# Kernel optimization log

Measured on AMD Instinct MI355X. Metric: run time of the kernel, lower is better.

## Reference

```python
import jax, jax.numpy as jnp
import numpy as np

B, K, C, Q, NCLS = 16, 36, 2048, 1024, 16
LIN = 1024
DIN = 2 * C + 16 + Q  # 5136


def _linear_params(key, din, dout, scale=0.02):
    kw, kb = jax.random.split(key)
    W = jax.random.normal(kw, (din, dout), dtype=jnp.float32) * scale
    b = jax.random.normal(kb, (dout,), dtype=jnp.float32) * scale
    return W, b


def setup_inputs() -> dict:
    key = jax.random.key(0)
    ks = jax.random.split(key, 12)
    box_feats = jax.random.normal(ks[0], (B, K, C), dtype=jnp.float32)
    q_feats = jax.random.normal(ks[1], (B, Q), dtype=jnp.float32)
    # valid boxes: x2>x1, y2>y1 so areas are strictly positive (no div-by-zero)
    x1y1 = jax.random.uniform(ks[2], (B, K, 2), dtype=jnp.float32)
    wh = jax.random.uniform(ks[3], (B, K, 2), dtype=jnp.float32, minval=0.05, maxval=1.0)
    box_coords = jnp.concatenate([x1y1, x1y1 + wh, wh], axis=-1)  # [B,K,6]
    index = jax.random.randint(ks[4], (B,), 1, K + 1)  # ragged box counts in [1,K]
    wholefeat = jax.random.normal(ks[5], (B, C), dtype=jnp.float32)
    pooled = jax.random.normal(ks[6], (B, C), dtype=jnp.float32)
    W1, b1 = _linear_params(ks[7], DIN, LIN)
    W2, b2 = _linear_params(ks[8], LIN, LIN)
    W3, b3 = _linear_params(ks[9], LIN, LIN)
    Wf1, bf1 = _linear_params(ks[10], LIN, LIN // 2)
    Wf2, bf2 = _linear_params(ks[11], LIN // 2, NCLS)
    return {"wholefeat": wholefeat, "pooled": pooled, "box_feats": box_feats,
            "q_feats": q_feats, "box_coords": box_coords, "index": index,
            "W1": W1, "b1": b1, "W2": W2, "b2": b2, "W3": W3, "b3": b3,
            "Wf1": Wf1, "bf1": bf1, "Wf2": Wf2, "bf2": bf2}


def _rn_forward(box_feats, q_feats, box_coords, index,
                W1, b1, W2, b2, W3, b3, Wf1, bf1, Wf2, bf2):
    b_, k_, c_ = box_feats.shape
    # ragged -> padded + mask: pair (i,j) valid iff i < index[b] and j < index[b]
    valid = (jnp.arange(k_)[None, :] < index[:, None]).astype(box_feats.dtype)  # [B,K]
    pair_mask = valid[:, :, None] * valid[:, None, :]  # [B,K,K]

    # pairwise dot of region features
    dot = jnp.einsum('bid,bjd->bij', box_feats, box_feats)[..., None]  # [B,K,K,1]

    bc = box_coords  # [B,K,6]
    area = (bc[..., 2] - bc[..., 0]) * (bc[..., 3] - bc[..., 1])  # [B,K]
    lr = jnp.maximum(0.0, jnp.minimum(bc[:, :, None, 2], bc[:, None, :, 2])
                     - jnp.maximum(bc[:, :, None, 0], bc[:, None, :, 0]))
    ud = jnp.maximum(0.0, jnp.minimum(bc[:, :, None, 3], bc[:, None, :, 3])
                     - jnp.maximum(bc[:, :, None, 1], bc[:, None, :, 1]))
    overlap = lr * ud  # [B,K,K]
    area_i = area[:, :, None]
    area_j = area[:, None, :]
    iou = (overlap / (area_i + area_j - overlap))[..., None]
    o_ij = (overlap / area_i)[..., None]
    o_ji = (overlap / area_j)[..., None]

    b_ij = jnp.broadcast_to(bc[:, :, None, :], (b_, k_, k_, 6))
    b_ji = jnp.broadcast_to(bc[:, None, :, :], (b_, k_, k_, 6))
    o_i = jnp.broadcast_to(box_feats[:, :, None, :], (b_, k_, k_, c_))
    o_j = jnp.broadcast_to(box_feats[:, None, :, :], (b_, k_, k_, c_))
    qst = jnp.broadcast_to(q_feats[:, None, None, :], (b_, k_, k_, q_feats.shape[-1]))

    # [B,K,K,5136] = [o_i, o_j, qst, dot, b_ij, b_ji, iou, o_ij, o_ji]
    feat = jnp.concatenate([o_i, o_j, qst, dot, b_ij, b_ji, iou, o_ij, o_ji], axis=-1)

    h = jax.nn.relu(feat @ W1 + b1)
    h = jax.nn.relu(h @ W2 + b2)
    h = jax.nn.relu(h @ W3 + b3)  # [B,K,K,1024]

    # masked sum-pool over all valid (i,j) pairs
    g = jnp.einsum('bijh,bij->bh', h, pair_mask)  # [B,1024]

    out = jax.nn.relu(g @ Wf1 + bf1) @ Wf2 + bf2  # [B,Ncls]
    return out


def reference(wholefeat, pooled, box_feats, q_feats, box_coords, index,
              W1, b1, W2, b2, W3, b3, Wf1, bf1, Wf2, bf2):
    # wholefeat / pooled are unused by the original forward as well
    return _rn_forward(box_feats, q_feats, box_coords, index,
                       W1, b1, W2, b2, W3, b3, Wf1, bf1, Wf2, bf2)
```

## Files before the change

kernel.cpp:

```cpp
#include <hip/hip_runtime.h>
#include <stdint.h>

typedef unsigned short u16;
typedef __attribute__((ext_vector_type(8))) short short8;
typedef __attribute__((ext_vector_type(4))) float f32x4;

#define Bn 16
#define Kn 36
#define Cn 2048
#define Qn 1024
#define LINn 1024
#define NPp 1296
#define NPAIRn 20736
#define NBIn 576

__device__ __forceinline__ u16 f2bf(float f) {
  union { float f; unsigned int u; } v; v.f = f;
  unsigned int r = v.u + 0x7FFFu + ((v.u >> 16) & 1u);
  return (u16)(r >> 16);
}

__device__ __forceinline__ void llds16(const void* g, void* l) {
  __builtin_amdgcn_global_load_lds((const __attribute__((address_space(1))) void*)g,
                                   (__attribute__((address_space(3))) void*)l, 16, 0, 0);
}

__global__ void k_transpose_all(const float* __restrict__ W1, const float* __restrict__ W2,
                                const float* __restrict__ W3, u16* __restrict__ W1abT,
                                u16* __restrict__ W2T, u16* __restrict__ W3T) {
  __shared__ float tile[32][33];
  int z = blockIdx.z;
  const float* src; u16* dst; int ld_dst;
  if (z == 0)      { if (blockIdx.y >= 32) return; src = W2; dst = W2T; ld_dst = 1024; }
  else if (z == 1) { if (blockIdx.y >= 32) return; src = W3; dst = W3T; ld_dst = 1024; }
  else if (z == 2) { src = W1; dst = W1abT; ld_dst = 2048; }
  else             { src = W1 + (size_t)2048 * 1024; dst = W1abT + (size_t)1024 * 2048; ld_dst = 2048; }
  int n0 = blockIdx.x * 32, k0 = blockIdx.y * 32;
  int tx = threadIdx.x & 31, ty = threadIdx.x >> 5;
#pragma unroll
  for (int r = 0; r < 32; r += 8)
    tile[ty + r][tx] = src[(size_t)(k0 + ty + r) * 1024 + (n0 + tx)];
  __syncthreads();
#pragma unroll
  for (int r = 0; r < 32; r += 8)
    dst[(size_t)(n0 + ty + r) * ld_dst + (k0 + tx)] = f2bf(tile[tx][ty + r]);
}

__global__ void k_f2b(const float4* __restrict__ src, ushort4* __restrict__ dst, int n4) {
  int i = blockIdx.x * 256 + threadIdx.x;
  if (i < n4) {
    float4 v = src[i];
    ushort4 o;
    o.x = f2bf(v.x); o.y = f2bf(v.y); o.z = f2bf(v.z); o.w = f2bf(v.w);
    dst[i] = o;
  }
}

__global__ void k_build(const int* __restrict__ index, int* __restrict__ pairList,
                        int* __restrict__ batchC, int* __restrict__ cnt2) {
  __shared__ int offs[17];
  int tid = threadIdx.x;
  if (tid == 0) {
    int o = 0;
    for (int b = 0; b < Bn; ++b) { offs[b] = o; int v = index[b]; o += v * v; }
    offs[16] = o;
    cnt2[0] = o;
    cnt2[1] = (o + 127) & ~127;
  }
  __syncthreads();
  int total = offs[16];
  int totalPad = (total + 127) & ~127;
  for (int b = 0; b < Bn; ++b) {
    int v = index[b]; int n = v * v; int base = offs[b];
    for (int t = tid; t < n; t += 256) {
      int i = t / v, j = t - i * v;
      pairList[base + t] = b * NPp + i * Kn + j;
      batchC[base + t] = b;
    }
  }
  for (int t = total + tid; t < totalPad; t += 256) {
    pairList[t] = 0;
    batchC[t] = 0;
  }
}

__global__ void k_pcinit(const float* __restrict__ b1, float* __restrict__ Pc) {
  int n = blockIdx.x * 256 + threadIdx.x;
  float v = b1[n];
#pragma unroll
  for (int b = 0; b < Bn; ++b) Pc[b * LINn + n] = v;
}

__global__ void k_pconst(const float* __restrict__ q, const float* __restrict__ W1,
                         float* __restrict__ Pc) {
  __shared__ float qs[Bn][32];
  int n = blockIdx.x * 256 + threadIdx.x;
  int k0 = blockIdx.y * 32;
  const float* Wq = W1 + (size_t)(2 * Cn) * LINn;
  for (int t = threadIdx.x; t < Bn * 32; t += 256) {
    int b = t >> 5, k = t & 31;
    qs[b][k] = q[b * Qn + k0 + k];
  }
  __syncthreads();
  float acc[Bn];
#pragma unroll
  for (int b = 0; b < Bn; ++b) acc[b] = 0.f;
  for (int k = 0; k < 32; ++k) {
    float w = Wq[(size_t)(k0 + k) * LINn + n];
#pragma unroll
    for (int b = 0; b < Bn; ++b) acc[b] += qs[b][k] * w;
  }
#pragma unroll
  for (int b = 0; b < Bn; ++b) atomicAdd(&Pc[b * LINn + n], acc[b]);
}

__global__ void k_pairscalars(const float* __restrict__ bfm, const float* __restrict__ bc,
                              const int* __restrict__ pairList, const int* __restrict__ cnt2,
                              float* __restrict__ dotC, float* __restrict__ iouC,
                              float* __restrict__ oijC, float* __restrict__ ojiC) {
  int cnt = cnt2[0];
  int lane = threadIdx.x & 63;
  for (int m = blockIdx.x * 4 + (threadIdx.x >> 6); m < cnt; m += gridDim.x * 4) {
    int p = pairList[m];
    int b = p / NPp, rem = p - b * NPp, i = rem / Kn, j = rem - (rem / Kn) * Kn;
    const float4* Ai = (const float4*)(bfm + (size_t)(b * Kn + i) * Cn);
    const float4* Aj = (const float4*)(bfm + (size_t)(b * Kn + j) * Cn);
    float s = 0.f;
#pragma unroll
    for (int t = 0; t < Cn / 4 / 64; ++t) {
      float4 x = Ai[lane + t * 64], y = Aj[lane + t * 64];
      s += x.x * y.x + x.y * y.y + x.z * y.z + x.w * y.w;
    }
#pragma unroll
    for (int o = 32; o > 0; o >>= 1) s += __shfl_down(s, o);
    if (lane == 0) {
      const float* ci = bc + (size_t)(b * Kn + i) * 6;
      const float* cj = bc + (size_t)(b * Kn + j) * 6;
      float ai = (ci[2] - ci[0]) * (ci[3] - ci[1]);
      float aj = (cj[2] - cj[0]) * (cj[3] - cj[1]);
      float lr = fmaxf(0.f, fminf(ci[2], cj[2]) - fmaxf(ci[0], cj[0]));
      float ud = fmaxf(0.f, fminf(ci[3], cj[3]) - fmaxf(ci[1], cj[1]));
      float ov = lr * ud;
      dotC[m] = s;
      iouC[m] = ov / (ai + aj - ov);
      oijC[m] = ov / ai;
      ojiC[m] = ov / aj;
    }
  }
}

__global__ void k_padd(const float* __restrict__ P12s, const float* __restrict__ Pc,
                       const float* __restrict__ bc, const float* __restrict__ W1,
                       float* __restrict__ P12) {
  int bi = blockIdx.x;
  int b = bi / Kn;
  const float* c = bc + (size_t)bi * 6;
  const float* W = W1 + (size_t)(2 * Cn + Qn + 1) * LINn;
  const size_t SL = (size_t)640 * 2048;
#pragma unroll
  for (int it = 0; it < 8; ++it) {
    int cc = it * 256 + threadIdx.x;
    size_t idx = (size_t)bi * 2048 + cc;
    float s = P12s[idx] + P12s[SL + idx] + P12s[2 * SL + idx] + P12s[3 * SL + idx];
    int n = cc & 1023;
    int rbase = (cc < 1024) ? 0 : 6;
    float a = 0.f;
#pragma unroll
    for (int t = 0; t < 6; ++t) a += c[t] * W[(size_t)(rbase + t) * LINn + n];
    if (cc < 1024) a += Pc[b * LINn + n];
    P12[idx] = s + a;
  }
}

__global__ void k_h1(const float* __restrict__ P12,
                     const float* __restrict__ dotC, const float* __restrict__ iouC,
                     const float* __restrict__ oijC, const float* __restrict__ ojiC,
                     const int* __restrict__ pairList, const int* __restrict__ cnt2,
                     const float* __restrict__ W1, u16* __restrict__ H1) {
  int cnt = cnt2[0];
  int t = threadIdx.x;
  const float4* wd = (const float4*)(W1 + (size_t)(2 * Cn + Qn) * LINn);
  const float4* wu = (const float4*)(W1 + (size_t)(2 * Cn + Qn + 13) * LINn);
  const float4* wa = (const float4*)(W1 + (size_t)(2 * Cn + Qn + 14) * LINn);
  const float4* wb = (const float4*)(W1 + (size_t)(2 * Cn + Qn + 15) * LINn);
  float4 e1 = wd[t], e2 = wu[t], e3 = wa[t], e4 = wb[t];
  for (int m = blockIdx.x; m < cnt; m += gridDim.x) {
    int p = pairList[m];
    int b = p / NPp, rem = p - b * NPp, i = rem / Kn, j = rem - (rem / Kn) * Kn;
    float d = dotC[m], u = iouC[m], o1 = oijC[m], o2 = ojiC[m];
    const float4* p1 = (const float4*)(P12 + (size_t)(b * Kn + i) * 2048);
    const float4* p2 = (const float4*)(P12 + (size_t)(b * Kn + j) * 2048 + 1024);
    ushort4* outp = (ushort4*)(H1 + (size_t)m * 1024);
    float4 v1 = p1[t], v2 = p2[t];
    ushort4 o;
    o.x = f2bf(fmaxf(v1.x + v2.x + d * e1.x + u * e2.x + o1 * e3.x + o2 * e4.x, 0.f));
    o.y = f2bf(fmaxf(v1.y + v2.y + d * e1.y + u * e2.y + o1 * e3.y + o2 * e4.y, 0.f));
    o.z = f2bf(fmaxf(v1.z + v2.z + d * e1.z + u * e2.z + o1 * e3.z + o2 * e4.z, 0.f));
    o.w = f2bf(fmaxf(v1.w + v2.w + d * e1.w + u * e2.w + o1 * e3.w + o2 * e4.w, 0.f));
    outp[t] = o;
  }
}

template <int EPI>
__global__ void __launch_bounds__(256) k_gemm(
    const u16* __restrict__ A, const u16* __restrict__ BT,
    int N, int K, int KC, int Mvalid, const int* __restrict__ cnt2,
    float* __restrict__ Cf, int CfSlice, u16* __restrict__ Cb,
    const float* __restrict__ bias,
    const int* __restrict__ batchC, float* __restrict__ G) {
  __shared__ u16 Alds[2][128 * 32];
  __shared__ u16 Blds[2][64 * 32];
  __shared__ float Gpart[(EPI == 2) ? (Bn * 64) : 4];

  const int tid = threadIdx.x;
  const int wave = tid >> 6, lane = tid & 63;
  const int wm = (wave >> 1) * 64, wn = (wave & 1) * 32;

  int Mv = Mvalid;
  int m0, n0;
  if (EPI == 0) {
    m0 = blockIdx.x * 128;
    n0 = blockIdx.y * 64;
  } else {
    Mv = cnt2[0];
    int nMt = (Mv + 127) >> 7;
    int nact = nMt * 16;
    int id = blockIdx.x;
    if (id >= nact) return;
    int q = nact >> 3, r = nact & 7;
    int xcd = id & 7, rank = id >> 3;
    int wg = (xcd < r ? xcd * (q + 1) : r * (q + 1) + (xcd - r) * q) + rank;
    m0 = (wg >> 4) * 128;
    n0 = (wg & 15) * 64;
  }
  if (EPI == 2) {
    for (int t = tid; t < Bn * 64; t += 256) Gpart[t] = 0.f;
  }

  f32x4 zero = {0.f, 0.f, 0.f, 0.f};
  f32x4 acc[4][2];
#pragma unroll
  for (int x = 0; x < 4; ++x)
#pragma unroll
    for (int y = 0; y < 2; ++y) acc[x][y] = zero;

  const int arow = tid >> 2;
  const int sslot = ((tid & 3) ^ ((tid >> 3) & 3)) * 16;
  const size_t ldb = (size_t)K * 2;

  auto stage = [&](int buf, int k0) {
    char* aB = (char*)Alds[buf] + wave * 1024;
    char* bB = (char*)Blds[buf] + wave * 1024;
#pragma unroll
    for (int c = 0; c < 2; ++c) {
      int rg = m0 + c * 64 + arow; if (rg >= Mv) rg = Mv - 1;
      llds16((const char*)A + (size_t)rg * ldb + (size_t)k0 * 2 + sslot, aB + c * 4096);
    }
    int rg = n0 + arow;
    llds16((const char*)BT + (size_t)rg * ldb + (size_t)k0 * 2 + sslot, bB);
  };

  auto compute = [&](int buf) {
    const char* Ab = (const char*)Alds[buf];
    const char* Bb = (const char*)Blds[buf];
    short8 af[4], bfr[2];
#pragma unroll
    for (int f = 0; f < 4; ++f) {
      int rA = wm + f * 16 + (lane & 15);
      int sl = ((lane >> 4) ^ ((rA >> 1) & 3)) * 16;
      af[f] = *(const short8*)(Ab + (size_t)rA * 64 + sl);
    }
#pragma unroll
    for (int f = 0; f < 2; ++f) {
      int rB = wn + f * 16 + (lane & 15);
      int sl = ((lane >> 4) ^ ((rB >> 1) & 3)) * 16;
      bfr[f] = *(const short8*)(Bb + (size_t)rB * 64 + sl);
    }
#pragma unroll
    for (int x = 0; x < 4; ++x)
#pragma unroll
      for (int y = 0; y < 2; ++y)
        acc[x][y] = __builtin_amdgcn_mfma_f32_16x16x32_bf16(af[x], bfr[y],
                                                            acc[x][y], 0, 0, 0);
  };

  const int kbeg = blockIdx.z * KC;
  const int nt = KC >> 5;
  stage(0, kbeg);
  for (int t = 0; t < nt; ++t) {
    if (t + 1 < nt) {
      stage((t + 1) & 1, kbeg + (t + 1) * 32);
      asm volatile("s_waitcnt vmcnt(3)" ::: "memory");
    } else {
      asm volatile("s_waitcnt vmcnt(0)" ::: "memory");
    }
    __builtin_amdgcn_s_barrier();
    compute(t & 1);
    __builtin_amdgcn_s_barrier();
  }

  if (EPI == 0) {
    float* Cs = Cf + (size_t)blockIdx.z * CfSlice;
#pragma unroll
    for (int x = 0; x < 4; ++x) {
      int rb = m0 + wm + x * 16 + (lane >> 4) * 4;
#pragma unroll
      for (int r = 0; r < 4; ++r) {
        int row = rb + r;
        if (row < Mv) {
#pragma unroll
          for (int y = 0; y < 2; ++y)
            Cs[(size_t)row * N + (n0 + wn + y * 16 + (lane & 15))] = acc[x][y][r];
        }
      }
    }
  } else if (EPI == 1) {
#pragma unroll
    for (int x = 0; x < 4; ++x) {
      int rb = m0 + wm + x * 16 + (lane >> 4) * 4;
#pragma unroll
      for (int r = 0; r < 4; ++r) {
        int row = rb + r;
#pragma unroll
        for (int y = 0; y < 2; ++y) {
          int col = n0 + wn + y * 16 + (lane & 15);
          Cb[(size_t)row * N + col] = f2bf(fmaxf(acc[x][y][r] + bias[col], 0.f));
        }
      }
    }
  } else {
    const int cnt = Mv;
#pragma unroll
    for (int x = 0; x < 4; ++x) {
      int rb = m0 + wm + x * 16 + (lane >> 4) * 4;
      int b0 = batchC[rb], b1 = batchC[rb + 1], b2 = batchC[rb + 2], b3 = batchC[rb + 3];
      float mk0 = (rb     < cnt) ? 1.f : 0.f;
      float mk1 = (rb + 1 < cnt) ? 1.f : 0.f;
      float mk2 = (rb + 2 < cnt) ? 1.f : 0.f;
      float mk3 = (rb + 3 < cnt) ? 1.f : 0.f;
#pragma unroll
      for (int y = 0; y < 2; ++y) {
        int coll = wn + y * 16 + (lane & 15);
        float bs = bias[n0 + coll];
        float s0 = mk0 * fmaxf(acc[x][y][0] + bs, 0.f);
        float s1 = mk1 * fmaxf(acc[x][y][1] + bs, 0.f);
        float s2 = mk2 * fmaxf(acc[x][y][2] + bs, 0.f);
        float s3 = mk3 * fmaxf(acc[x][y][3] + bs, 0.f);
        if (b0 == b3) {
          atomicAdd(&Gpart[b0 * 64 + coll], s0 + s1 + s2 + s3);
        } else {
          atomicAdd(&Gpart[b0 * 64 + coll], s0);
          atomicAdd(&Gpart[b1 * 64 + coll], s1);
          atomicAdd(&Gpart[b2 * 64 + coll], s2);
          atomicAdd(&Gpart[b3 * 64 + coll], s3);
        }
      }
    }
    __syncthreads();
    for (int t2 = tid; t2 < Bn * 64; t2 += 256) {
      float v = Gpart[t2];
      if (v != 0.f) atomicAdd(&G[(t2 >> 6) * LINn + n0 + (t2 & 63)], v);
    }
  }
}

__global__ void k_final1(const float* __restrict__ G, const float* __restrict__ Wf1,
                         float* __restrict__ S) {
  __shared__ float g[128];
  int b = blockIdx.x, kz = blockIdx.y, tid = threadIdx.x;
  if (tid < 128) g[tid] = G[b * 1024 + kz * 128 + tid];
  __syncthreads();
  float acc = 0.f;
  const float* W = Wf1 + (size_t)(kz * 128) * 512 + tid;
  for (int k = 0; k < 128; ++k) acc += g[k] * W[(size_t)k * 512];
  atomicAdd(&S[b * 512 + tid], acc);
}

__global__ void k_final2(const float* __restrict__ S, const float* __restrict__ bf1,
                         const float* __restrict__ Wf2, const float* __restrict__ bf2,
                         float* __restrict__ out) {
  __shared__ float mid[512];
  __shared__ float part[256];
  int b = blockIdx.x, tid = threadIdx.x;
  for (int t = tid; t < 512; t += 256) mid[t] = fmaxf(S[b * 512 + t] + bf1[t], 0.f);
  __syncthreads();
  int o = tid & 15, seg = tid >> 4;
  float s = 0.f;
#pragma unroll
  for (int t = 0; t < 32; ++t) {
    int j = seg * 32 + t;
    s += mid[j] * Wf2[j * 16 + o];
  }
  part[tid] = s;
  __syncthreads();
  if (tid < 16) {
    float v = bf2[tid];
#pragma unroll
    for (int sg = 0; sg < 16; ++sg) v += part[sg * 16 + tid];
    out[b * 16 + tid] = v;
  }
}

extern "C" void kernel_launch(void* const* d_in, const int* in_sizes, int n_in,
                              void* d_out, int out_size, void* d_ws, size_t ws_size,
                              hipStream_t stream) {
  const float* box_feats  = (const float*)d_in[2];
  const float* q_feats    = (const float*)d_in[3];
  const float* box_coords = (const float*)d_in[4];
  const int*   index      = (const int*)d_in[5];
  const float* W1  = (const float*)d_in[6];
  const float* b1  = (const float*)d_in[7];
  const float* W2  = (const float*)d_in[8];
  const float* b2  = (const float*)d_in[9];
  const float* W3  = (const float*)d_in[10];
  const float* b3  = (const float*)d_in[11];
  const float* Wf1 = (const float*)d_in[12];
  const float* bf1 = (const float*)d_in[13];
  const float* Wf2 = (const float*)d_in[14];
  const float* bf2 = (const float*)d_in[15];
  float* out = (float*)d_out;

  char* ws = (char*)d_ws;
  size_t off = 0;
  auto alloc = [&](size_t bytes) { void* p = ws + off; off += (bytes + 255) & ~(size_t)255; return p; };
  u16* W1abT = (u16*)alloc((size_t)2048 * 2048 * 2);
  u16* W2T   = (u16*)alloc((size_t)1024 * 1024 * 2);
  u16* W3T   = (u16*)alloc((size_t)1024 * 1024 * 2);
  u16* BFb   = (u16*)alloc((size_t)NBIn * Cn * 2);
  float* P12s = (float*)alloc((size_t)4 * 640 * 2048 * 4);
  float* P12  = (float*)alloc((size_t)NBIn * 2048 * 4);
  float* Pc   = (float*)alloc((size_t)Bn * LINn * 4);
  float* dotC = (float*)alloc((size_t)NPAIRn * 4);
  float* iouC = (float*)alloc((size_t)NPAIRn * 4);
  float* oijC = (float*)alloc((size_t)NPAIRn * 4);
  float* ojiC = (float*)alloc((size_t)NPAIRn * 4);
  int* pairList = (int*)alloc((size_t)NPAIRn * 4);
  int* batchC   = (int*)alloc((size_t)NPAIRn * 4);
  int* cnt2     = (int*)alloc(64);
  float* G  = (float*)alloc((size_t)Bn * LINn * 4);
  float* S  = (float*)alloc((size_t)Bn * 512 * 4);
  u16* H1 = (u16*)alloc((size_t)NPAIRn * 1024 * 2);
  u16* H2 = (u16*)alloc((size_t)NPAIRn * 1024 * 2);

  k_transpose_all<<<dim3(32, 64, 4), 256, 0, stream>>>(W1, W2, W3, W1abT, W2T, W3T);
  k_f2b<<<(NBIn * Cn / 4 + 255) / 256, 256, 0, stream>>>((const float4*)box_feats,
                                                         (ushort4*)BFb, NBIn * Cn / 4);
  k_build<<<1, 256, 0, stream>>>(index, pairList, batchC, cnt2);
  k_pcinit<<<4, 256, 0, stream>>>(b1, Pc);
  k_pconst<<<dim3(4, 32), 256, 0, stream>>>(q_feats, W1, Pc);
  k_pairscalars<<<648, 256, 0, stream>>>(box_feats, box_coords, pairList, cnt2,
                                         dotC, iouC, oijC, ojiC);
  k_gemm<0><<<dim3(5, 32, 4), 256, 0, stream>>>(BFb, W1abT, 2048, 2048, 512, NBIn, nullptr,
                                                P12s, 640 * 2048, nullptr, nullptr,
                                                nullptr, nullptr);
  k_padd<<<NBIn, 256, 0, stream>>>(P12s, Pc, box_coords, W1, P12);
  k_h1<<<2592, 256, 0, stream>>>(P12, dotC, iouC, oijC, ojiC, pairList, cnt2, W1, H1);
  hipMemsetAsync(G, 0, (size_t)Bn * LINn * 4, stream);
  hipMemsetAsync(S, 0, (size_t)Bn * 512 * 4, stream);
  k_gemm<1><<<dim3(2592, 1, 1), 256, 0, stream>>>(H1, W2T, 1024, 1024, 1024, 0, cnt2,
                                                  nullptr, 0, H2, b2, nullptr, nullptr);
  k_gemm<2><<<dim3(2592, 1, 1), 256, 0, stream>>>(H2, W3T, 1024, 1024, 1024, 0, cnt2,
                                                  nullptr, 0, nullptr, b3, batchC, G);
  k_final1<<<dim3(16, 8), 512, 0, stream>>>(G, Wf1, S);
  k_final2<<<16, 256, 0, stream>>>(S, bf1, Wf2, bf2, out);
}
```

Baseline: 159.3 us.

## Fuse second and third MLP GEMMs into one kernel keeping activations in LDS

Replaces the two separate GEMM launches for layers 2 and 3 with one kernel. Each 512-thread block holds a 64-row tile of H1 in LDS (128KB), computes all 1024 output columns of layer 2, writes the ReLU'd bf16 result back into the same LDS tile, then runs layer 3 and sum-pools straight into G with global atomics. This removes the H2 round trip through HBM and one launch. In exchange, weight B-fragments are loaded directly from global memory without LDS staging, each block gets only 64 rows of reuse, per-thread accumulator pressure is high, and the shared-LDS partial reduction is replaced by direct global atomics.

```diff
diff --git a/kernel.cpp b/kernel.cpp
--- a/kernel.cpp
+++ b/kernel.cpp
@@ -201,41 +201,18 @@
   }
 }
 
-template <int EPI>
-__global__ void __launch_bounds__(256) k_gemm(
+__global__ void __launch_bounds__(256) k_gemmP(
     const u16* __restrict__ A, const u16* __restrict__ BT,
-    int N, int K, int KC, int Mvalid, const int* __restrict__ cnt2,
-    float* __restrict__ Cf, int CfSlice, u16* __restrict__ Cb,
-    const float* __restrict__ bias,
-    const int* __restrict__ batchC, float* __restrict__ G) {
+    int N, int K, int KC, int Mvalid,
+    float* __restrict__ Cf, int CfSlice) {
   __shared__ u16 Alds[2][128 * 32];
   __shared__ u16 Blds[2][64 * 32];
-  __shared__ float Gpart[(EPI == 2) ? (Bn * 64) : 4];
-
   const int tid = threadIdx.x;
   const int wave = tid >> 6, lane = tid & 63;
   const int wm = (wave >> 1) * 64, wn = (wave & 1) * 32;
-
-  int Mv = Mvalid;
-  int m0, n0;
-  if (EPI == 0) {
-    m0 = blockIdx.x * 128;
-    n0 = blockIdx.y * 64;
-  } else {
-    Mv = cnt2[0];
-    int nMt = (Mv + 127) >> 7;
-    int nact = nMt * 16;
-    int id = blockIdx.x;
-    if (id >= nact) return;
-    int q = nact >> 3, r = nact & 7;
-    int xcd = id & 7, rank = id >> 3;
-    int wg = (xcd < r ? xcd * (q + 1) : r * (q + 1) + (xcd - r) * q) + rank;
-    m0 = (wg >> 4) * 128;
-    n0 = (wg & 15) * 64;
-  }
-  if (EPI == 2) {
-    for (int t = tid; t < Bn * 64; t += 256) Gpart[t] = 0.f;
-  }
+  const int m0 = blockIdx.x * 128;
+  const int n0 = blockIdx.y * 64;
+  const int Mv = Mvalid;
 
   f32x4 zero = {0.f, 0.f, 0.f, 0.f};
   f32x4 acc[4][2];
@@ -299,67 +276,152 @@
     __builtin_amdgcn_s_barrier();
   }
 
-  if (EPI == 0) {
-    float* Cs = Cf + (size_t)blockIdx.z * CfSlice;
-#pragma unroll
-    for (int x = 0; x < 4; ++x) {
-      int rb = m0 + wm + x * 16 + (lane >> 4) * 4;
+  float* Cs = Cf + (size_t)blockIdx.z * CfSlice;
+#pragma unroll
+  for (int x = 0; x < 4; ++x) {
+    int rb = m0 + wm + x * 16 + (lane >> 4) * 4;
+#pragma unroll
+    for (int r = 0; r < 4; ++r) {
+      int row = rb + r;
+      if (row < Mv) {
+#pragma unroll
+        for (int y = 0; y < 2; ++y)
+          Cs[(size_t)row * N + (n0 + wn + y * 16 + (lane & 15))] = acc[x][y][r];
+      }
+    }
+  }
+}
+
+__global__ void __launch_bounds__(512, 2) k_fused23(
+    const u16* __restrict__ H1, const u16* __restrict__ W2T, const u16* __restrict__ W3T,
+    const float* __restrict__ b2, const float* __restrict__ b3,
+    const int* __restrict__ batchC, const int* __restrict__ cnt2,
+    float* __restrict__ G) {
+  __shared__ u16 T[64][1024];
+  const int tid = threadIdx.x;
+  const int wave = tid >> 6, lane = tid & 63;
+  const int cnt = cnt2[0];
+  const int r0g = blockIdx.x * 64;
+  if (r0g >= cnt) return;
+  const int cw = wave * 128;
+
+#pragma unroll
+  for (int rd = 0; rd < 16; ++rd) {
+    int row = rd * 4 + (wave >> 1);
+    int s0 = (wave & 1) << 6;
+    int gr = r0g + row; if (gr >= cnt) gr = cnt - 1;
+    int sslot = (s0 + lane) ^ (row & 7);
+    llds16(H1 + (size_t)gr * 1024 + (size_t)sslot * 8, &T[row][s0 * 8]);
+  }
+  __syncthreads();
+
+  f32x4 zero = {0.f, 0.f, 0.f, 0.f};
+  f32x4 acc[4][8];
+#pragma unroll
+  for (int x = 0; x < 4; ++x)
+#pragma unroll
+    for (int y = 0; y < 8; ++y) acc[x][y] = zero;
+
+  float bias[8];
+#pragma unroll
+  for (int y = 0; y < 8; ++y) bias[y] = b2[cw + y * 16 + (lane & 15)];
+
+#pragma unroll 2
+  for (int k0 = 0; k0 < 1024; k0 += 64) {
+#pragma unroll
+    for (int kk = 0; kk < 2; ++kk) {
+      int ksl = (k0 >> 3) + kk * 4 + (lane >> 4);
+      short8 af[4];
+#pragma unroll
+      for (int x = 0; x < 4; ++x) {
+        int row = x * 16 + (lane & 15);
+        af[x] = *(const short8*)&T[row][(ksl ^ (row & 7)) << 3];
+      }
+      const u16* wp = W2T + k0 + kk * 32 + ((lane >> 4) << 3);
+      short8 bf[8];
+#pragma unroll
+      for (int y = 0; y < 8; ++y)
+        bf[y] = *(const short8*)(wp + (size_t)(cw + y * 16 + (lane & 15)) * 1024);
+#pragma unroll
+      for (int x = 0; x < 4; ++x)
+#pragma unroll
+        for (int y = 0; y < 8; ++y)
+          acc[x][y] = __builtin_amdgcn_mfma_f32_16x16x32_bf16(af[x], bf[y],
+                                                              acc[x][y], 0, 0, 0);
+    }
+  }
+
+  __syncthreads();
+#pragma unroll
+  for (int x = 0; x < 4; ++x) {
+    int rbase = x * 16 + ((lane >> 4) << 2);
+#pragma unroll
+    for (int y = 0; y < 8; ++y) {
+      int col = cw + y * 16 + (lane & 15);
 #pragma unroll
       for (int r = 0; r < 4; ++r) {
-        int row = rb + r;
-        if (row < Mv) {
-#pragma unroll
-          for (int y = 0; y < 2; ++y)
-            Cs[(size_t)row * N + (n0 + wn + y * 16 + (lane & 15))] = acc[x][y][r];
-        }
+        int row = rbase + r;
+        float v = fmaxf(acc[x][y][r] + bias[y], 0.f);
+        T[row][((((col >> 3) ^ (row & 7)) << 3) | (col & 7))] = f2bf(v);
       }
-    }
-  } else if (EPI == 1) {
-#pragma unroll
-    for (int x = 0; x < 4; ++x) {
-      int rb = m0 + wm + x * 16 + (lane >> 4) * 4;
-#pragma unroll
-      for (int r = 0; r < 4; ++r) {
-        int row = rb + r;
-#pragma unroll
-        for (int y = 0; y < 2; ++y) {
-          int col = n0 + wn + y * 16 + (lane & 15);
-          Cb[(size_t)row * N + col] = f2bf(fmaxf(acc[x][y][r] + bias[col], 0.f));
-        }
+      acc[x][y] = zero;
+    }
+  }
+  __syncthreads();
+
+#pragma unroll
+  for (int y = 0; y < 8; ++y) bias[y] = b3[cw + y * 16 + (lane & 15)];
+
+#pragma unroll 2
+  for (int k0 = 0; k0 < 1024; k0 += 64) {
+#pragma unroll
+    for (int kk = 0; kk < 2; ++kk) {
+      int ksl = (k0 >> 3) + kk * 4 + (lane >> 4);
+      short8 af[4];
+#pragma unroll
+      for (int x = 0; x < 4; ++x) {
+        int row = x * 16 + (lane & 15);
+        af[x] = *(const short8*)&T[row][(ksl ^ (row & 7)) << 3];
       }
-    }
-  } else {
-    const int cnt = Mv;
-#pragma unroll
-    for (int x = 0; x < 4; ++x) {
-      int rb = m0 + wm + x * 16 + (lane >> 4) * 4;
-      int b0 = batchC[rb], b1 = batchC[rb + 1], b2 = batchC[rb + 2], b3 = batchC[rb + 3];
-      float mk0 = (rb     < cnt) ? 1.f : 0.f;
-      float mk1 = (rb + 1 < cnt) ? 1.f : 0.f;
-      float mk2 = (rb + 2 < cnt) ? 1.f : 0.f;
-      float mk3 = (rb + 3 < cnt) ? 1.f : 0.f;
-#pragma unroll
-      for (int y = 0; y < 2; ++y) {
-        int coll = wn + y * 16 + (lane & 15);
-        float bs = bias[n0 + coll];
-        float s0 = mk0 * fmaxf(acc[x][y][0] + bs, 0.f);
-        float s1 = mk1 * fmaxf(acc[x][y][1] + bs, 0.f);
-        float s2 = mk2 * fmaxf(acc[x][y][2] + bs, 0.f);
-        float s3 = mk3 * fmaxf(acc[x][y][3] + bs, 0.f);
-        if (b0 == b3) {
-          atomicAdd(&Gpart[b0 * 64 + coll], s0 + s1 + s2 + s3);
-        } else {
-          atomicAdd(&Gpart[b0 * 64 + coll], s0);
-          atomicAdd(&Gpart[b1 * 64 + coll], s1);
-          atomicAdd(&Gpart[b2 * 64 + coll], s2);
-          atomicAdd(&Gpart[b3 * 64 + coll], s3);
-        }
+      const u16* wp = W3T + k0 + kk * 32 + ((lane >> 4) << 3);
+      short8 bf[8];
+#pragma unroll
+      for (int y = 0; y < 8; ++y)
+        bf[y] = *(const short8*)(wp + (size_t)(cw + y * 16 + (lane & 15)) * 1024);
+#pragma unroll
+      for (int x = 0; x < 4; ++x)
+#pragma unroll
+        for (int y = 0; y < 8; ++y)
+          acc[x][y] = __builtin_amdgcn_mfma_f32_16x16x32_bf16(af[x], bf[y],
+                                                              acc[x][y], 0, 0, 0);
+    }
+  }
+
+#pragma unroll
+  for (int x = 0; x < 4; ++x) {
+    int gr = r0g + x * 16 + ((lane >> 4) << 2);
+    int bb0, bb1, bb2, bb3;
+    float mk0, mk1, mk2, mk3;
+    bb0 = batchC[(gr     < cnt) ? gr     : (cnt - 1)]; mk0 = (gr     < cnt) ? 1.f : 0.f;
+    bb1 = batchC[(gr + 1 < cnt) ? gr + 1 : (cnt - 1)]; mk1 = (gr + 1 < cnt) ? 1.f : 0.f;
+    bb2 = batchC[(gr + 2 < cnt) ? gr + 2 : (cnt - 1)]; mk2 = (gr + 2 < cnt) ? 1.f : 0.f;
+    bb3 = batchC[(gr + 3 < cnt) ? gr + 3 : (cnt - 1)]; mk3 = (gr + 3 < cnt) ? 1.f : 0.f;
+#pragma unroll
+    for (int y = 0; y < 8; ++y) {
+      int col = cw + y * 16 + (lane & 15);
+      float bs = bias[y];
+      float s0 = mk0 * fmaxf(acc[x][y][0] + bs, 0.f);
+      float s1 = mk1 * fmaxf(acc[x][y][1] + bs, 0.f);
+      float s2 = mk2 * fmaxf(acc[x][y][2] + bs, 0.f);
+      float s3 = mk3 * fmaxf(acc[x][y][3] + bs, 0.f);
+      if (bb0 == bb3) {
+        atomicAdd(&G[bb0 * LINn + col], s0 + s1 + s2 + s3);
+      } else {
+        atomicAdd(&G[bb0 * LINn + col], s0);
+        atomicAdd(&G[bb1 * LINn + col], s1);
+        atomicAdd(&G[bb2 * LINn + col], s2);
+        atomicAdd(&G[bb3 * LINn + col], s3);
       }
-    }
-    __syncthreads();
-    for (int t2 = tid; t2 < Bn * 64; t2 += 256) {
-      float v = Gpart[t2];
-      if (v != 0.f) atomicAdd(&G[(t2 >> 6) * LINn + n0 + (t2 & 63)], v);
     }
   }
 }
@@ -440,7 +502,6 @@
   float* G  = (float*)alloc((size_t)Bn * LINn * 4);
   float* S  = (float*)alloc((size_t)Bn * 512 * 4);
   u16* H1 = (u16*)alloc((size_t)NPAIRn * 1024 * 2);
-  u16* H2 = (u16*)alloc((size_t)NPAIRn * 1024 * 2);
 
   k_transpose_all<<<dim3(32, 64, 4), 256, 0, stream>>>(W1, W2, W3, W1abT, W2T, W3T);
   k_f2b<<<(NBIn * Cn / 4 + 255) / 256, 256, 0, stream>>>((const float4*)box_feats,
@@ -450,17 +511,13 @@
   k_pconst<<<dim3(4, 32), 256, 0, stream>>>(q_feats, W1, Pc);
   k_pairscalars<<<648, 256, 0, stream>>>(box_feats, box_coords, pairList, cnt2,
                                          dotC, iouC, oijC, ojiC);
-  k_gemm<0><<<dim3(5, 32, 4), 256, 0, stream>>>(BFb, W1abT, 2048, 2048, 512, NBIn, nullptr,
-                                                P12s, 640 * 2048, nullptr, nullptr,
-                                                nullptr, nullptr);
+  k_gemmP<<<dim3(5, 32, 4), 256, 0, stream>>>(BFb, W1abT, 2048, 2048, 512, NBIn,
+                                              P12s, 640 * 2048);
   k_padd<<<NBIn, 256, 0, stream>>>(P12s, Pc, box_coords, W1, P12);
   k_h1<<<2592, 256, 0, stream>>>(P12, dotC, iouC, oijC, ojiC, pairList, cnt2, W1, H1);
   hipMemsetAsync(G, 0, (size_t)Bn * LINn * 4, stream);
   hipMemsetAsync(S, 0, (size_t)Bn * 512 * 4, stream);
-  k_gemm<1><<<dim3(2592, 1, 1), 256, 0, stream>>>(H1, W2T, 1024, 1024, 1024, 0, cnt2,
-                                                  nullptr, 0, H2, b2, nullptr, nullptr);
-  k_gemm<2><<<dim3(2592, 1, 1), 256, 0, stream>>>(H2, W3T, 1024, 1024, 1024, 0, cnt2,
-                                                  nullptr, 0, nullptr, b3, batchC, G);
+  k_fused23<<<324, 512, 0, stream>>>(H1, W2T, W3T, b2, b3, batchC, cnt2, G);
   k_final1<<<dim3(16, 8), 512, 0, stream>>>(G, Wf1, S);
   k_final2<<<16, 256, 0, stream>>>(S, bf1, Wf2, bf2, out);
 }
```

Result: slower. 279.0 us (+75.1%).
